# Performance work log

Measured on AMD Instinct MI355X. Metric: run time of the kernel, lower is better.

The kernel has to match this reference:

```python
import jax, jax.numpy as jnp
import numpy as np

B, N, D, H, E, K = 8, 4096, 128, 256, 16, 2


def setup_inputs() -> dict:
    key = jax.random.key(0)
    ks = jax.random.split(key, 11)
    sc = 0.05
    return {
        "x":   jax.random.normal(ks[0], (B, N, D), jnp.float32),
        "Wg":  jax.random.normal(ks[1], (D, E), jnp.float32) * sc,
        "bg":  jnp.zeros((E,), jnp.float32),
        "W1":  jax.random.normal(ks[2], (E, D, H), jnp.float32) * sc,
        "b1":  jnp.zeros((E, H), jnp.float32),
        "W2":  jax.random.normal(ks[3], (E, H, D), jnp.float32) * sc,
        "b2":  jnp.zeros((E, D), jnp.float32),
        "Wu1": jax.random.normal(ks[4], (D, H), jnp.float32) * sc,
        "bu1": jnp.zeros((H,), jnp.float32),
        "Wu2": jax.random.normal(ks[5], (H, D), jnp.float32) * sc,
        "bu2": jnp.zeros((D,), jnp.float32),
    }


def reference(x, Wg, bg, W1, b1, W2, b2, Wu1, bu1, Wu2, bu2):
    b, n, d = x.shape
    xt = x.reshape(b * n, d)                       # [T, D]
    T = xt.shape[0]

    # gating: top-k logits kept, rest -inf, then softmax -> zeros off top-k
    logits = xt @ Wg + bg                          # [T, E]
    topv, topi = jax.lax.top_k(logits, K)          # [T, K]
    mask = jnp.full_like(logits, -jnp.inf)
    mask = mask.at[jnp.arange(T)[:, None], topi].set(topv)
    gate = jax.nn.softmax(mask, axis=-1)           # [T, E]

    # dense all-expert MLP (matches original torch.stack over experts)
    h = jax.nn.relu(jnp.einsum('td,edh->teh', xt, W1) + b1)   # [T, E, H]
    eo = jnp.einsum('teh,ehd->ted', h, W2) + b2               # [T, E, D]

    # universal expert scaled by omega = 1 - max gate
    omega = 1.0 - jnp.max(gate, axis=1, keepdims=True)        # [T, 1]
    uni = omega * (jax.nn.relu(xt @ Wu1 + bu1) @ Wu2 + bu2)   # [T, D]

    out = jnp.einsum('te,ted->td', gate, eo) + uni
    return out.reshape(b, n, d)
```

## Files before the change

### kernel.cpp

```cpp
#include <hip/hip_runtime.h>
#include <hip/hip_bf16.h>

constexpr int kT = 32768;
constexpr int kD = 128;
constexpr int kH = 256;
constexpr int kE = 16;

typedef __bf16 bf16x8 __attribute__((ext_vector_type(8)));
typedef unsigned short u16x8 __attribute__((ext_vector_type(8)));
typedef float f32x4 __attribute__((ext_vector_type(4)));

#define LDX 136
#define LDQ 72

constexpr int NB_TP   = 272;
constexpr int NB_GATE = kT / 64;
constexpr int CNT_STRIDE = 32;
constexpr int MOE_GRID = 1552;

__device__ __forceinline__ unsigned short f2bf(float f) {
  unsigned int u = __float_as_uint(f);
  u += 0x7FFFu + ((u >> 16) & 1u);
  return (unsigned short)(u >> 16);
}
__device__ __forceinline__ float bf2f(unsigned short s) {
  return __uint_as_float((unsigned int)s << 16);
}
__device__ __forceinline__ void bar_lgkm() {
  asm volatile("s_waitcnt lgkmcnt(0)" ::: "memory");
  __builtin_amdgcn_s_barrier();
  asm volatile("" ::: "memory");
}

__global__ __launch_bounds__(256) void front_kernel(
    const float* __restrict__ x, const float* __restrict__ Wg,
    const float* __restrict__ bg,
    const float* __restrict__ W1, const float* __restrict__ W2,
    const float* __restrict__ Wu1, const float* __restrict__ Wu2,
    unsigned short* __restrict__ xb, unsigned short* __restrict__ W1t,
    unsigned short* __restrict__ W2t, unsigned short* __restrict__ Wu1t,
    unsigned short* __restrict__ Wu2t,
    int* __restrict__ cnt, int* __restrict__ btok, float* __restrict__ bgate,
    int* __restrict__ tpos)
{
  __shared__ __align__(16) char smem[46848];
  const int tid = threadIdx.x;
  const int b = blockIdx.x;

  if (b < NB_TP) {
    int bb = b;
    const float* src; unsigned short* dst; int R, C, r0, c0;
    if (bb < 136) {
      int m = bb >> 3, t8 = bb & 7;
      R = 128; C = 256;
      src = (m < 16) ? W1 + (size_t)m * 32768 : Wu1;
      dst = (m < 16) ? W1t + (size_t)m * 32768 : Wu1t;
      r0 = (t8 & 1) * 64; c0 = (t8 >> 1) * 64;
    } else {
      bb -= 136;
      int m = bb >> 3, t8 = bb & 7;
      R = 256; C = 128;
      src = (m < 16) ? W2 + (size_t)m * 32768 : Wu2;
      dst = (m < 16) ? W2t + (size_t)m * 32768 : Wu2t;
      r0 = (t8 >> 1) * 64; c0 = (t8 & 1) * 64;
    }
    unsigned short (*tl)[72] = reinterpret_cast<unsigned short(*)[72]>(smem);
#pragma unroll
    for (int i = 0; i < 4; ++i) {
      int s = i * 256 + tid;
      int r = s >> 4, c4 = s & 15;
      float4 v = *reinterpret_cast<const float4*>(&src[(size_t)(r0 + r) * C + c0 + c4 * 4]);
      tl[c4 * 4 + 0][r] = f2bf(v.x);
      tl[c4 * 4 + 1][r] = f2bf(v.y);
      tl[c4 * 4 + 2][r] = f2bf(v.z);
      tl[c4 * 4 + 3][r] = f2bf(v.w);
    }
    __syncthreads();
#pragma unroll
    for (int i = 0; i < 2; ++i) {
      int s = i * 256 + tid;
      int c = s >> 3, seg = s & 7;
      uint4 v = *reinterpret_cast<const uint4*>(&tl[c][seg * 8]);
      *reinterpret_cast<uint4*>(&dst[(size_t)(c0 + c) * R + r0 + seg * 8]) = v;
    }
    return;
  }

  {
    float* sWt = reinterpret_cast<float*>(smem);
    float* sX  = reinterpret_cast<float*>(smem + 8448);
    float* sL  = reinterpret_cast<float*>(smem + 42240);
    int* hcnt  = reinterpret_cast<int*>(smem + 46592);
    int* hbase = reinterpret_cast<int*>(smem + 46656);
    int* hb16  = reinterpret_cast<int*>(smem + 46720);
    const int t0 = (b - NB_TP) * 64;

    if (tid < kE) hcnt[tid] = 0;
    for (int i = tid; i < kD * kE; i += 256) {
      int d = i >> 4, e = i & 15;
      sWt[e * 132 + d] = Wg[i];
    }
    const float4* xv = reinterpret_cast<const float4*>(x + (size_t)t0 * kD);
    for (int i = tid; i < 64 * kD / 4; i += 256) {
      int r = i >> 5, c4 = i & 31;
      *reinterpret_cast<float4*>(&sX[r * 132 + c4 * 4]) = xv[i];
    }
    __syncthreads();

    const int e = tid & 15, tq = tid >> 4;
    const double bgd = (double)bg[e];
    const float4* wr = reinterpret_cast<const float4*>(&sWt[e * 132]);
    double acc[4] = {0.0, 0.0, 0.0, 0.0};
#pragma unroll
    for (int d4 = 0; d4 < 32; ++d4) {
      float4 wa = wr[d4];
#pragma unroll
      for (int p = 0; p < 4; ++p) {
        float4 xa = *reinterpret_cast<const float4*>(&sX[(p * 16 + tq) * 132 + d4 * 4]);
        acc[p] += (double)xa.x * (double)wa.x + (double)xa.y * (double)wa.y
                + (double)xa.z * (double)wa.z + (double)xa.w * (double)wa.w;
      }
    }
#pragma unroll
    for (int p = 0; p < 4; ++p)
      sL[(p * 16 + tq) * 17 + e] = (float)(acc[p] + bgd);
#pragma unroll
    for (int p = 0; p < 4; ++p) {
      int idx = p * 256 + tid;
      int r = idx >> 4, c8 = (idx & 15) * 8;
      const float* sp = &sX[r * 132 + c8];
      u16x8 v;
#pragma unroll
      for (int j = 0; j < 8; ++j) v[j] = f2bf(sp[j]);
      *reinterpret_cast<u16x8*>(&xb[(size_t)(t0 + r) * kD + c8]) = v;
    }
    __syncthreads();

    int e0 = 0, e1 = 0, lp0 = 0, lp1 = 0;
    float g0 = 0.f, g1 = 0.f;
    const int t = t0 + tid;
    if (tid < 64) {
      float v0 = -3.4e38f, v1 = -3.4e38f;
      for (int i = 0; i < kE; ++i) {
        float v = sL[tid * 17 + i];
        if (v > v0) { v1 = v0; e1 = e0; v0 = v; e0 = i; }
        else if (v > v1) { v1 = v; e1 = i; }
      }
      float r = expf(v1 - v0);
      g0 = 1.f / (1.f + r);
      g1 = 1.f - g0;
      lp0 = atomicAdd(&hcnt[e0], 1);
      lp1 = atomicAdd(&hcnt[e1], 1);
    }
    if (tid == 0) hb16[0] = atomicAdd(&cnt[16 * CNT_STRIDE], 64);
    __syncthreads();
    if (tid < kE)
      hbase[tid] = atomicAdd(&cnt[tid * CNT_STRIDE], hcnt[tid]);
    __syncthreads();
    if (tid < 64) {
      int p0 = hbase[e0] + lp0;
      btok[e0 * kT + p0] = t; bgate[e0 * kT + p0] = g0;
      int p1 = hbase[e1] + lp1;
      btok[e1 * kT + p1] = t; bgate[e1 * kT + p1] = g1;
      int p2 = hb16[0] + tid;
      btok[16 * kT + p2] = t; bgate[16 * kT + p2] = 1.f - g0;
      tpos[2 * t]     = (e0 << 16) | p0;
      tpos[2 * t + 1] = (e1 << 16) | p1;
    }
  }
}

#define LOAD_W1(BUF, HQ)                                                      \
  _Pragma("unroll")                                                           \
  for (int kk = 0; kk < 4; ++kk)                                              \
    W1r[BUF][kk] = *reinterpret_cast<const bf16x8*>(                          \
        Bw1 + (size_t)((HQ) * 64 + w * 16 + lr) * kD + kk * 32 + lg * 8);

#define LOAD_W2(BUF, HQ)                                                      \
  _Pragma("unroll")                                                           \
  for (int n = 0; n < 2; ++n)                                                 \
    _Pragma("unroll")                                                         \
    for (int k2 = 0; k2 < 2; ++k2)                                            \
      W2r[BUF][n * 2 + k2] = *reinterpret_cast<const bf16x8*>(                \
          Bw2 + (size_t)(w * 32 + n * 16 + lr) * kH + (HQ) * 64 + k2 * 32 + lg * 8);

__global__ __launch_bounds__(256) void moe_kernel(
    const unsigned short* __restrict__ xb,
    const unsigned short* __restrict__ W1t,
    const unsigned short* __restrict__ W2t,
    const unsigned short* __restrict__ Wu1t,
    const unsigned short* __restrict__ Wu2t,
    const float* __restrict__ b1, const float* __restrict__ b2,
    const float* __restrict__ bu1, const float* __restrict__ bu2,
    const int* __restrict__ cnt, const int* __restrict__ btok,
    const float* __restrict__ bgate,
    unsigned short* __restrict__ eo, float* __restrict__ out)
{
  __shared__ alignas(16) char smem[27136];
  unsigned short* xs = reinterpret_cast<unsigned short*>(smem);
  unsigned short* hs = reinterpret_cast<unsigned short*>(smem + 17408);
  int*   toks = reinterpret_cast<int*>(smem + 26624);
  float* gts  = reinterpret_cast<float*>(smem + 26880);
  unsigned short* stB = reinterpret_cast<unsigned short*>(smem);
  float* stF = reinterpret_cast<float*>(smem);
  const int tid = threadIdx.x;
  const int bid = blockIdx.x;

  int c17[17];
#pragma unroll
  for (int i = 0; i < 17; ++i) c17[i] = cnt[i * CNT_STRIDE];
  int e = -1, tile = 0, eobase = 0, accb = 0;
#pragma unroll
  for (int i = 0; i < 17; ++i) {
    int tl = (c17[i] + 63) >> 6;
    if (e < 0) {
      if (bid < accb + tl) { e = i; tile = bid - accb; }
      else { accb += tl; if (i < 16) eobase += c17[i]; }
    }
  }
  if (e < 0) return;
  const int rows = min(64, c17[e] - tile * 64);

  const int w = tid >> 6, l = tid & 63, lr = l & 15, lg = l >> 4;
  const int gr = tid >> 4, gc = (tid & 15) * 8;
  const f32x4 z4 = {0.f, 0.f, 0.f, 0.f};

  const unsigned short* Bw1 = (e < 16) ? W1t + (size_t)e * kH * kD : Wu1t;
  const unsigned short* Bw2 = (e < 16) ? W2t + (size_t)e * kD * kH : Wu2t;
  const float* bs1 = (e < 16) ? b1 + (size_t)e * kH : bu1;
  const float* bs2 = (e < 16) ? b2 + (size_t)e * kD : bu2;

  bf16x8 W1r[2][4], W2r[2][4];
  LOAD_W1(0, 0); LOAD_W2(0, 0);
  float b1q[4];
#pragma unroll
  for (int hq = 0; hq < 4; ++hq) b1q[hq] = bs1[hq * 64 + w * 16 + lr];
  float b2v[2];
#pragma unroll
  for (int n = 0; n < 2; ++n) b2v[n] = bs2[w * 32 + n * 16 + lr];

  {
    int tokR[4]; float gtR[4];
#pragma unroll
    for (int p = 0; p < 4; ++p) {
      int r = p * 16 + gr; bool v = r < rows; int bi2 = e * kT + tile * 64 + r;
      tokR[p] = v ? btok[bi2] : 0;
      gtR[p]  = v ? bgate[bi2] : 0.f;
    }
#pragma unroll
    for (int p = 0; p < 4; ++p) {
      uint4 v = *reinterpret_cast<const uint4*>(xb + (size_t)tokR[p] * kD + gc);
      *reinterpret_cast<uint4*>(&xs[(p * 16 + gr) * LDX + gc]) = v;
    }
    if ((tid & 15) == 0) {
#pragma unroll
      for (int p = 0; p < 4; ++p) {
        toks[p * 16 + gr] = tokR[p];
        gts[p * 16 + gr]  = gtR[p];
      }
    }
  }
  f32x4 acc2[4][2];
#pragma unroll
  for (int m = 0; m < 4; ++m)
#pragma unroll
    for (int n = 0; n < 2; ++n) acc2[m][n] = z4;
  bar_lgkm();

#pragma unroll
  for (int hq = 0; hq < 4; ++hq) {
    const int cur = hq & 1;
    if (hq < 3) {
      const int nxt = cur ^ 1;
      LOAD_W1(nxt, hq + 1);
      LOAD_W2(nxt, hq + 1);
    }
    f32x4 acc[4];
#pragma unroll
    for (int m = 0; m < 4; ++m) acc[m] = z4;
#pragma unroll
    for (int kk = 0; kk < 4; ++kk) {
      bf16x8 a[4];
#pragma unroll
      for (int m = 0; m < 4; ++m)
        a[m] = *reinterpret_cast<const bf16x8*>(xs + (m * 16 + lr) * LDX + kk * 32 + lg * 8);
#pragma unroll
      for (int m = 0; m < 4; ++m)
        acc[m] = __builtin_amdgcn_mfma_f32_16x16x32_bf16(a[m], W1r[cur][kk], acc[m], 0, 0, 0);
    }
#pragma unroll
    for (int m = 0; m < 4; ++m)
#pragma unroll
      for (int q = 0; q < 4; ++q) {
        float v = acc[m][q] + b1q[hq];
        v = fmaxf(v, 0.f);
        hs[(m * 16 + lg * 4 + q) * LDQ + w * 16 + lr] = f2bf(v);
      }
    bar_lgkm();
#pragma unroll
    for (int k2 = 0; k2 < 2; ++k2) {
      bf16x8 a[4];
#pragma unroll
      for (int m = 0; m < 4; ++m)
        a[m] = *reinterpret_cast<const bf16x8*>(hs + (m * 16 + lr) * LDQ + k2 * 32 + lg * 8);
#pragma unroll
      for (int m = 0; m < 4; ++m)
#pragma unroll
        for (int n = 0; n < 2; ++n)
          acc2[m][n] = __builtin_amdgcn_mfma_f32_16x16x32_bf16(a[m], W2r[cur][n * 2 + k2], acc2[m][n], 0, 0, 0);
    }
    bar_lgkm();
  }

  if (e < 16) {
#pragma unroll
    for (int m = 0; m < 4; ++m)
#pragma unroll
      for (int q = 0; q < 4; ++q) {
        int r = m * 16 + lg * 4 + q;
        float g = gts[r];
#pragma unroll
        for (int n = 0; n < 2; ++n)
          stB[r * LDX + w * 32 + n * 16 + lr] = f2bf(g * (acc2[m][n][q] + b2v[n]));
      }
    bar_lgkm();
    unsigned short* dst = eo + (size_t)(eobase + tile * 64) * kD;
#pragma unroll
    for (int j = 0; j < 4; ++j) {
      int gidx = j * 256 + tid;
      int r = gidx >> 4, seg = gidx & 15;
      if (r < rows) {
        uint4 v = *reinterpret_cast<const uint4*>(&stB[r * LDX + seg * 8]);
        *reinterpret_cast<uint4*>(dst + (size_t)r * kD + seg * 8) = v;
      }
    }
  } else {
#pragma unroll
    for (int ch = 0; ch < 2; ++ch) {
      if ((w >> 1) == ch) {
#pragma unroll
        for (int m = 0; m < 4; ++m)
#pragma unroll
          for (int q = 0; q < 4; ++q) {
            int r = m * 16 + lg * 4 + q;
            float g = gts[r];
#pragma unroll
            for (int n = 0; n < 2; ++n)
              stF[r * 68 + (w & 1) * 32 + n * 16 + lr] = g * (acc2[m][n][q] + b2v[n]);
          }
      }
      bar_lgkm();
#pragma unroll
      for (int j = 0; j < 4; ++j) {
        int gidx = j * 256 + tid;
        int r = gidx >> 4, seg = gidx & 15;
        if (r < rows) {
          int tok = toks[r];
          float4 v = *reinterpret_cast<const float4*>(&stF[r * 68 + seg * 4]);
          *reinterpret_cast<float4*>(out + (size_t)tok * kD + ch * 64 + seg * 4) = v;
        }
      }
      bar_lgkm();
    }
  }
}

__global__ __launch_bounds__(256) void combine_kernel(
    const int* __restrict__ cnt, const int* __restrict__ tpos,
    const unsigned short* __restrict__ eo, float* __restrict__ out)
{
  __shared__ int base[16];
  const int tid = threadIdx.x;
  if (tid < 16) {
    int s = 0;
    for (int i = 0; i < tid; ++i) s += cnt[i * CNT_STRIDE];
    base[tid] = s;
  }
  __syncthreads();
  const int tk = blockIdx.x * 16 + (tid >> 4);
  const int c = tid & 15;
  int a0 = tpos[2 * tk], a1 = tpos[2 * tk + 1];
  size_t r0 = (size_t)(base[a0 >> 16] + (a0 & 0xffff)) * kD + c * 8;
  size_t r1 = (size_t)(base[a1 >> 16] + (a1 & 0xffff)) * kD + c * 8;
  u16x8 v0 = *reinterpret_cast<const u16x8*>(eo + r0);
  u16x8 v1 = *reinterpret_cast<const u16x8*>(eo + r1);
  float s[8];
#pragma unroll
  for (int j = 0; j < 8; ++j) s[j] = bf2f(v0[j]) + bf2f(v1[j]);
  float4* op = reinterpret_cast<float4*>(out + (size_t)tk * kD + c * 8);
  float4 o0 = op[0], o1 = op[1];
  o0.x += s[0]; o0.y += s[1]; o0.z += s[2]; o0.w += s[3];
  o1.x += s[4]; o1.y += s[5]; o1.z += s[6]; o1.w += s[7];
  op[0] = o0; op[1] = o1;
}

extern "C" void kernel_launch(void* const* d_in, const int* in_sizes, int n_in,
                              void* d_out, int out_size, void* d_ws, size_t ws_size,
                              hipStream_t stream) {
  (void)in_sizes; (void)n_in; (void)out_size; (void)ws_size;
  const float* x   = (const float*)d_in[0];
  const float* Wg  = (const float*)d_in[1];
  const float* bg  = (const float*)d_in[2];
  const float* W1  = (const float*)d_in[3];
  const float* b1  = (const float*)d_in[4];
  const float* W2  = (const float*)d_in[5];
  const float* b2  = (const float*)d_in[6];
  const float* Wu1 = (const float*)d_in[7];
  const float* bu1 = (const float*)d_in[8];
  const float* Wu2 = (const float*)d_in[9];
  const float* bu2 = (const float*)d_in[10];
  float* out = (float*)d_out;

  char* ws = (char*)d_ws;
  constexpr size_t OFF_XB    = 0;
  constexpr size_t OFF_W1T   = 8388608;
  constexpr size_t OFF_W2T   = 9437184;
  constexpr size_t OFF_WU1T  = 10485760;
  constexpr size_t OFF_WU2T  = 10551296;
  constexpr size_t OFF_CNT   = 10616832;
  constexpr size_t OFF_TPOS  = 10620928;
  constexpr size_t OFF_BTOK  = 10883072;
  constexpr size_t OFF_BGATE = 13111296;
  constexpr size_t OFF_EO    = 15339520;

  unsigned short* xb   = (unsigned short*)(ws + OFF_XB);
  unsigned short* W1t  = (unsigned short*)(ws + OFF_W1T);
  unsigned short* W2t  = (unsigned short*)(ws + OFF_W2T);
  unsigned short* Wu1t = (unsigned short*)(ws + OFF_WU1T);
  unsigned short* Wu2t = (unsigned short*)(ws + OFF_WU2T);
  int*   cnt   = (int*)(ws + OFF_CNT);
  int*   tpos  = (int*)(ws + OFF_TPOS);
  int*   btok  = (int*)(ws + OFF_BTOK);
  float* bgate = (float*)(ws + OFF_BGATE);
  unsigned short* eo = (unsigned short*)(ws + OFF_EO);

  hipMemsetAsync(cnt, 0, 17 * CNT_STRIDE * sizeof(int), stream);
  front_kernel<<<NB_TP + NB_GATE, 256, 0, stream>>>(
      x, Wg, bg, W1, W2, Wu1, Wu2,
      xb, W1t, W2t, Wu1t, Wu2t, cnt, btok, bgate, tpos);
  moe_kernel<<<MOE_GRID, 256, 0, stream>>>(
      xb, W1t, W2t, Wu1t, Wu2t, b1, b2, bu1, bu2, cnt, btok, bgate, eo, out);
  combine_kernel<<<kT / 16, 256, 0, stream>>>(cnt, tpos, eo, out);
}
```

Measured before the change: 76.06 us.

## Swap MFMA operands for transposed accumulators and remap block ids across XCDs

Swaps the A/B operands of both MFMA GEMMs so each lane's accumulator holds four consecutive columns of one row instead of four rows of one column. The bias adds, ReLU and bf16/f32 writes to shared memory become single vectorized 8- or 16-byte stores per fragment instead of scalar stores. Bias loads become f32x4 vector loads, and the gate is read once per m-tile. Block ids are also permuted so that consecutive work tiles, which share expert weights, land on the same XCD for better L2 reuse; this assumes the grid size is divisible by 8.

```diff
diff --git a/kernel.cpp b/kernel.cpp
--- a/kernel.cpp
+++ b/kernel.cpp
@@ -8,6 +8,7 @@
 
 typedef __bf16 bf16x8 __attribute__((ext_vector_type(8)));
 typedef unsigned short u16x8 __attribute__((ext_vector_type(8)));
+typedef unsigned short u16x4 __attribute__((ext_vector_type(4)));
 typedef float f32x4 __attribute__((ext_vector_type(4)));
 
 #define LDX 136
@@ -204,7 +205,7 @@
   unsigned short* stB = reinterpret_cast<unsigned short*>(smem);
   float* stF = reinterpret_cast<float*>(smem);
   const int tid = threadIdx.x;
-  const int bid = blockIdx.x;
+  const int bid = (blockIdx.x & 7) * (MOE_GRID / 8) + (blockIdx.x >> 3);
 
   int c17[17];
 #pragma unroll
@@ -232,12 +233,13 @@
 
   bf16x8 W1r[2][4], W2r[2][4];
   LOAD_W1(0, 0); LOAD_W2(0, 0);
-  float b1q[4];
-#pragma unroll
-  for (int hq = 0; hq < 4; ++hq) b1q[hq] = bs1[hq * 64 + w * 16 + lr];
-  float b2v[2];
-#pragma unroll
-  for (int n = 0; n < 2; ++n) b2v[n] = bs2[w * 32 + n * 16 + lr];
+  f32x4 b1s[4], b2s[2];
+#pragma unroll
+  for (int hq = 0; hq < 4; ++hq)
+    b1s[hq] = *reinterpret_cast<const f32x4*>(bs1 + hq * 64 + w * 16 + lg * 4);
+#pragma unroll
+  for (int n = 0; n < 2; ++n)
+    b2s[n] = *reinterpret_cast<const f32x4*>(bs2 + w * 32 + n * 16 + lg * 4);
 
   {
     int tokR[4]; float gtR[4];
@@ -286,16 +288,16 @@
         a[m] = *reinterpret_cast<const bf16x8*>(xs + (m * 16 + lr) * LDX + kk * 32 + lg * 8);
 #pragma unroll
       for (int m = 0; m < 4; ++m)
-        acc[m] = __builtin_amdgcn_mfma_f32_16x16x32_bf16(a[m], W1r[cur][kk], acc[m], 0, 0, 0);
-    }
-#pragma unroll
-    for (int m = 0; m < 4; ++m)
-#pragma unroll
-      for (int q = 0; q < 4; ++q) {
-        float v = acc[m][q] + b1q[hq];
-        v = fmaxf(v, 0.f);
-        hs[(m * 16 + lg * 4 + q) * LDQ + w * 16 + lr] = f2bf(v);
-      }
+        acc[m] = __builtin_amdgcn_mfma_f32_16x16x32_bf16(W1r[cur][kk], a[m], acc[m], 0, 0, 0);
+    }
+#pragma unroll
+    for (int m = 0; m < 4; ++m) {
+      u16x4 hv;
+#pragma unroll
+      for (int q = 0; q < 4; ++q)
+        hv[q] = f2bf(fmaxf(acc[m][q] + b1s[hq][q], 0.f));
+      *reinterpret_cast<u16x4*>(&hs[(m * 16 + lr) * LDQ + w * 16 + lg * 4]) = hv;
+    }
     bar_lgkm();
 #pragma unroll
     for (int k2 = 0; k2 < 2; ++k2) {
@@ -307,22 +309,24 @@
       for (int m = 0; m < 4; ++m)
 #pragma unroll
         for (int n = 0; n < 2; ++n)
-          acc2[m][n] = __builtin_amdgcn_mfma_f32_16x16x32_bf16(a[m], W2r[cur][n * 2 + k2], acc2[m][n], 0, 0, 0);
+          acc2[m][n] = __builtin_amdgcn_mfma_f32_16x16x32_bf16(W2r[cur][n * 2 + k2], a[m], acc2[m][n], 0, 0, 0);
     }
     bar_lgkm();
   }
 
   if (e < 16) {
 #pragma unroll
-    for (int m = 0; m < 4; ++m)
-#pragma unroll
-      for (int q = 0; q < 4; ++q) {
-        int r = m * 16 + lg * 4 + q;
-        float g = gts[r];
-#pragma unroll
-        for (int n = 0; n < 2; ++n)
-          stB[r * LDX + w * 32 + n * 16 + lr] = f2bf(g * (acc2[m][n][q] + b2v[n]));
-      }
+    for (int m = 0; m < 4; ++m) {
+      float g = gts[m * 16 + lr];
+#pragma unroll
+      for (int n = 0; n < 2; ++n) {
+        u16x4 sv;
+#pragma unroll
+        for (int q = 0; q < 4; ++q)
+          sv[q] = f2bf(g * (acc2[m][n][q] + b2s[n][q]));
+        *reinterpret_cast<u16x4*>(&stB[(m * 16 + lr) * LDX + w * 32 + n * 16 + lg * 4]) = sv;
+      }
+    }
     bar_lgkm();
     unsigned short* dst = eo + (size_t)(eobase + tile * 64) * kD;
 #pragma unroll
@@ -339,15 +343,17 @@
     for (int ch = 0; ch < 2; ++ch) {
       if ((w >> 1) == ch) {
 #pragma unroll
-        for (int m = 0; m < 4; ++m)
-#pragma unroll
-          for (int q = 0; q < 4; ++q) {
-            int r = m * 16 + lg * 4 + q;
-            float g = gts[r];
-#pragma unroll
-            for (int n = 0; n < 2; ++n)
-              stF[r * 68 + (w & 1) * 32 + n * 16 + lr] = g * (acc2[m][n][q] + b2v[n]);
+        for (int m = 0; m < 4; ++m) {
+          float g = gts[m * 16 + lr];
+#pragma unroll
+          for (int n = 0; n < 2; ++n) {
+            f32x4 sv;
+#pragma unroll
+            for (int q = 0; q < 4; ++q)
+              sv[q] = g * (acc2[m][n][q] + b2s[n][q]);
+            *reinterpret_cast<f32x4*>(&stF[(m * 16 + lr) * 68 + (w & 1) * 32 + n * 16 + lg * 4]) = sv;
           }
+        }
       }
       bar_lgkm();
 #pragma unroll
```

Measured after the change: 79.71 us. 4.8% more time.

## Split universal expert into its own kernel fused with the combine step

Applied to the files above, without the earlier changes.

The universal expert moves out of the routed MoE kernel into a new kernel that processes contiguous 64-token tiles. That kernel computes omega-scaled universal MLP output and adds the two gathered expert rows before writing out directly. This removes the separate combine kernel's read-modify-write of the fp32 output and the scattered writes of the universal-expert path. The trade-off is one extra omega buffer and a smaller expert grid, while keeping three launches in total.

```diff
diff --git a/kernel.cpp b/kernel.cpp
--- a/kernel.cpp
+++ b/kernel.cpp
@@ -8,6 +8,7 @@
 
 typedef __bf16 bf16x8 __attribute__((ext_vector_type(8)));
 typedef unsigned short u16x8 __attribute__((ext_vector_type(8)));
+typedef unsigned short u16x4 __attribute__((ext_vector_type(4)));
 typedef float f32x4 __attribute__((ext_vector_type(4)));
 
 #define LDX 136
@@ -16,7 +17,7 @@
 constexpr int NB_TP   = 272;
 constexpr int NB_GATE = kT / 64;
 constexpr int CNT_STRIDE = 32;
-constexpr int MOE_GRID = 1552;
+constexpr int EXP_GRID = 1040;
 
 __device__ __forceinline__ unsigned short f2bf(float f) {
   unsigned int u = __float_as_uint(f);
@@ -41,7 +42,7 @@
     unsigned short* __restrict__ W2t, unsigned short* __restrict__ Wu1t,
     unsigned short* __restrict__ Wu2t,
     int* __restrict__ cnt, int* __restrict__ btok, float* __restrict__ bgate,
-    int* __restrict__ tpos)
+    int* __restrict__ tpos, float* __restrict__ omega)
 {
   __shared__ __align__(16) char smem[46848];
   const int tid = threadIdx.x;
@@ -92,7 +93,6 @@
     float* sL  = reinterpret_cast<float*>(smem + 42240);
     int* hcnt  = reinterpret_cast<int*>(smem + 46592);
     int* hbase = reinterpret_cast<int*>(smem + 46656);
-    int* hb16  = reinterpret_cast<int*>(smem + 46720);
     const int t0 = (b - NB_TP) * 64;
 
     if (tid < kE) hcnt[tid] = 0;
@@ -149,10 +149,10 @@
       float r = expf(v1 - v0);
       g0 = 1.f / (1.f + r);
       g1 = 1.f - g0;
+      omega[t] = 1.f - g0;
       lp0 = atomicAdd(&hcnt[e0], 1);
       lp1 = atomicAdd(&hcnt[e1], 1);
     }
-    if (tid == 0) hb16[0] = atomicAdd(&cnt[16 * CNT_STRIDE], 64);
     __syncthreads();
     if (tid < kE)
       hbase[tid] = atomicAdd(&cnt[tid * CNT_STRIDE], hcnt[tid]);
@@ -162,8 +162,6 @@
       btok[e0 * kT + p0] = t; bgate[e0 * kT + p0] = g0;
       int p1 = hbase[e1] + lp1;
       btok[e1 * kT + p1] = t; bgate[e1 * kT + p1] = g1;
-      int p2 = hb16[0] + tid;
-      btok[16 * kT + p2] = t; bgate[16 * kT + p2] = 1.f - g0;
       tpos[2 * t]     = (e0 << 16) | p0;
       tpos[2 * t + 1] = (e1 << 16) | p1;
     }
@@ -184,17 +182,14 @@
       W2r[BUF][n * 2 + k2] = *reinterpret_cast<const bf16x8*>(                \
           Bw2 + (size_t)(w * 32 + n * 16 + lr) * kH + (HQ) * 64 + k2 * 32 + lg * 8);
 
-__global__ __launch_bounds__(256) void moe_kernel(
+__global__ __launch_bounds__(256) void moe_expert_kernel(
     const unsigned short* __restrict__ xb,
     const unsigned short* __restrict__ W1t,
     const unsigned short* __restrict__ W2t,
-    const unsigned short* __restrict__ Wu1t,
-    const unsigned short* __restrict__ Wu2t,
     const float* __restrict__ b1, const float* __restrict__ b2,
-    const float* __restrict__ bu1, const float* __restrict__ bu2,
     const int* __restrict__ cnt, const int* __restrict__ btok,
     const float* __restrict__ bgate,
-    unsigned short* __restrict__ eo, float* __restrict__ out)
+    unsigned short* __restrict__ eo)
 {
   __shared__ alignas(16) char smem[27136];
   unsigned short* xs = reinterpret_cast<unsigned short*>(smem);
@@ -202,33 +197,32 @@
   int*   toks = reinterpret_cast<int*>(smem + 26624);
   float* gts  = reinterpret_cast<float*>(smem + 26880);
   unsigned short* stB = reinterpret_cast<unsigned short*>(smem);
-  float* stF = reinterpret_cast<float*>(smem);
   const int tid = threadIdx.x;
   const int bid = blockIdx.x;
 
-  int c17[17];
-#pragma unroll
-  for (int i = 0; i < 17; ++i) c17[i] = cnt[i * CNT_STRIDE];
+  int c16[16];
+#pragma unroll
+  for (int i = 0; i < 16; ++i) c16[i] = cnt[i * CNT_STRIDE];
   int e = -1, tile = 0, eobase = 0, accb = 0;
 #pragma unroll
-  for (int i = 0; i < 17; ++i) {
-    int tl = (c17[i] + 63) >> 6;
+  for (int i = 0; i < 16; ++i) {
+    int tl = (c16[i] + 63) >> 6;
     if (e < 0) {
       if (bid < accb + tl) { e = i; tile = bid - accb; }
-      else { accb += tl; if (i < 16) eobase += c17[i]; }
+      else { accb += tl; eobase += c16[i]; }
     }
   }
   if (e < 0) return;
-  const int rows = min(64, c17[e] - tile * 64);
+  const int rows = min(64, c16[e] - tile * 64);
 
   const int w = tid >> 6, l = tid & 63, lr = l & 15, lg = l >> 4;
   const int gr = tid >> 4, gc = (tid & 15) * 8;
   const f32x4 z4 = {0.f, 0.f, 0.f, 0.f};
 
-  const unsigned short* Bw1 = (e < 16) ? W1t + (size_t)e * kH * kD : Wu1t;
-  const unsigned short* Bw2 = (e < 16) ? W2t + (size_t)e * kD * kH : Wu2t;
-  const float* bs1 = (e < 16) ? b1 + (size_t)e * kH : bu1;
-  const float* bs2 = (e < 16) ? b2 + (size_t)e * kD : bu2;
+  const unsigned short* Bw1 = W1t + (size_t)e * kH * kD;
+  const unsigned short* Bw2 = W2t + (size_t)e * kD * kH;
+  const float* bs1 = b1 + (size_t)e * kH;
+  const float* bs2 = b2 + (size_t)e * kD;
 
   bf16x8 W1r[2][4], W2r[2][4];
   LOAD_W1(0, 0); LOAD_W2(0, 0);
@@ -312,86 +306,160 @@
     bar_lgkm();
   }
 
-  if (e < 16) {
+#pragma unroll
+  for (int m = 0; m < 4; ++m)
+#pragma unroll
+    for (int q = 0; q < 4; ++q) {
+      int r = m * 16 + lg * 4 + q;
+      float g = gts[r];
+#pragma unroll
+      for (int n = 0; n < 2; ++n)
+        stB[r * LDX + w * 32 + n * 16 + lr] = f2bf(g * (acc2[m][n][q] + b2v[n]));
+    }
+  bar_lgkm();
+  unsigned short* dst = eo + (size_t)(eobase + tile * 64) * kD;
+#pragma unroll
+  for (int j = 0; j < 4; ++j) {
+    int gidx = j * 256 + tid;
+    int r = gidx >> 4, seg = gidx & 15;
+    if (r < rows) {
+      uint4 v = *reinterpret_cast<const uint4*>(&stB[r * LDX + seg * 8]);
+      *reinterpret_cast<uint4*>(dst + (size_t)r * kD + seg * 8) = v;
+    }
+  }
+}
+
+__global__ __launch_bounds__(256) void uni_combine_kernel(
+    const unsigned short* __restrict__ xb,
+    const unsigned short* __restrict__ Wu1t,
+    const unsigned short* __restrict__ Wu2t,
+    const float* __restrict__ bu1, const float* __restrict__ bu2,
+    const float* __restrict__ omega, const int* __restrict__ cnt,
+    const int* __restrict__ tpos, const unsigned short* __restrict__ eo,
+    float* __restrict__ out)
+{
+  __shared__ alignas(16) char smem[27456];
+  unsigned short* xs = reinterpret_cast<unsigned short*>(smem);
+  unsigned short* hs = reinterpret_cast<unsigned short*>(smem + 17408);
+  float* sOm  = reinterpret_cast<float*>(smem + 26624);
+  int*   sTp  = reinterpret_cast<int*>(smem + 26880);
+  int*   sBase= reinterpret_cast<int*>(smem + 27392);
+  float* stF  = reinterpret_cast<float*>(smem);
+  const int tid = threadIdx.x;
+  const int t0 = blockIdx.x * 64;
+
+  const int w = tid >> 6, l = tid & 63, lr = l & 15, lg = l >> 4;
+  const int gr = tid >> 4, gc = (tid & 15) * 8;
+  const f32x4 z4 = {0.f, 0.f, 0.f, 0.f};
+
+  const unsigned short* Bw1 = Wu1t;
+  const unsigned short* Bw2 = Wu2t;
+  bf16x8 W1r[2][4], W2r[2][4];
+  LOAD_W1(0, 0); LOAD_W2(0, 0);
+  float b1q[4];
+#pragma unroll
+  for (int hq = 0; hq < 4; ++hq) b1q[hq] = bu1[hq * 64 + w * 16 + lr];
+  float b2v[2];
+#pragma unroll
+  for (int n = 0; n < 2; ++n) b2v[n] = bu2[w * 32 + n * 16 + lr];
+
+  if (tid < 16) {
+    int s = 0;
+    for (int i = 0; i < tid; ++i) s += cnt[i * CNT_STRIDE];
+    sBase[tid] = s;
+  }
+  if (tid >= 64 && tid < 128) sOm[tid - 64] = omega[t0 + tid - 64];
+  if (tid >= 128) sTp[tid - 128] = tpos[2 * t0 + tid - 128];
+#pragma unroll
+  for (int p = 0; p < 4; ++p) {
+    uint4 v = *reinterpret_cast<const uint4*>(xb + (size_t)(t0 + p * 16 + gr) * kD + gc);
+    *reinterpret_cast<uint4*>(&xs[(p * 16 + gr) * LDX + gc]) = v;
+  }
+  f32x4 acc2[4][2];
+#pragma unroll
+  for (int m = 0; m < 4; ++m)
+#pragma unroll
+    for (int n = 0; n < 2; ++n) acc2[m][n] = z4;
+  bar_lgkm();
+
+#pragma unroll
+  for (int hq = 0; hq < 4; ++hq) {
+    const int cur = hq & 1;
+    if (hq < 3) {
+      const int nxt = cur ^ 1;
+      LOAD_W1(nxt, hq + 1);
+      LOAD_W2(nxt, hq + 1);
+    }
+    f32x4 acc[4];
+#pragma unroll
+    for (int m = 0; m < 4; ++m) acc[m] = z4;
+#pragma unroll
+    for (int kk = 0; kk < 4; ++kk) {
+      bf16x8 a[4];
+#pragma unroll
+      for (int m = 0; m < 4; ++m)
+        a[m] = *reinterpret_cast<const bf16x8*>(xs + (m * 16 + lr) * LDX + kk * 32 + lg * 8);
+#pragma unroll
+      for (int m = 0; m < 4; ++m)
+        acc[m] = __builtin_amdgcn_mfma_f32_16x16x32_bf16(a[m], W1r[cur][kk], acc[m], 0, 0, 0);
+    }
 #pragma unroll
     for (int m = 0; m < 4; ++m)
 #pragma unroll
       for (int q = 0; q < 4; ++q) {
-        int r = m * 16 + lg * 4 + q;
-        float g = gts[r];
-#pragma unroll
-        for (int n = 0; n < 2; ++n)
-          stB[r * LDX + w * 32 + n * 16 + lr] = f2bf(g * (acc2[m][n][q] + b2v[n]));
+        float v = acc[m][q] + b1q[hq];
+        v = fmaxf(v, 0.f);
+        hs[(m * 16 + lg * 4 + q) * LDQ + w * 16 + lr] = f2bf(v);
       }
     bar_lgkm();
-    unsigned short* dst = eo + (size_t)(eobase + tile * 64) * kD;
+#pragma unroll
+    for (int k2 = 0; k2 < 2; ++k2) {
+      bf16x8 a[4];
+#pragma unroll
+      for (int m = 0; m < 4; ++m)
+        a[m] = *reinterpret_cast<const bf16x8*>(hs + (m * 16 + lr) * LDQ + k2 * 32 + lg * 8);
+#pragma unroll
+      for (int m = 0; m < 4; ++m)
+#pragma unroll
+        for (int n = 0; n < 2; ++n)
+          acc2[m][n] = __builtin_amdgcn_mfma_f32_16x16x32_bf16(a[m], W2r[cur][n * 2 + k2], acc2[m][n], 0, 0, 0);
+    }
+    bar_lgkm();
+  }
+
+#pragma unroll
+  for (int ch = 0; ch < 2; ++ch) {
+    if ((w >> 1) == ch) {
+#pragma unroll
+      for (int m = 0; m < 4; ++m)
+#pragma unroll
+        for (int q = 0; q < 4; ++q) {
+          int r = m * 16 + lg * 4 + q;
+          float om = sOm[r];
+#pragma unroll
+          for (int n = 0; n < 2; ++n)
+            stF[r * 68 + (w & 1) * 32 + n * 16 + lr] = om * (acc2[m][n][q] + b2v[n]);
+        }
+    }
+    bar_lgkm();
 #pragma unroll
     for (int j = 0; j < 4; ++j) {
       int gidx = j * 256 + tid;
       int r = gidx >> 4, seg = gidx & 15;
-      if (r < rows) {
-        uint4 v = *reinterpret_cast<const uint4*>(&stB[r * LDX + seg * 8]);
-        *reinterpret_cast<uint4*>(dst + (size_t)r * kD + seg * 8) = v;
-      }
-    }
-  } else {
-#pragma unroll
-    for (int ch = 0; ch < 2; ++ch) {
-      if ((w >> 1) == ch) {
-#pragma unroll
-        for (int m = 0; m < 4; ++m)
-#pragma unroll
-          for (int q = 0; q < 4; ++q) {
-            int r = m * 16 + lg * 4 + q;
-            float g = gts[r];
-#pragma unroll
-            for (int n = 0; n < 2; ++n)
-              stF[r * 68 + (w & 1) * 32 + n * 16 + lr] = g * (acc2[m][n][q] + b2v[n]);
-          }
-      }
-      bar_lgkm();
-#pragma unroll
-      for (int j = 0; j < 4; ++j) {
-        int gidx = j * 256 + tid;
-        int r = gidx >> 4, seg = gidx & 15;
-        if (r < rows) {
-          int tok = toks[r];
-          float4 v = *reinterpret_cast<const float4*>(&stF[r * 68 + seg * 4]);
-          *reinterpret_cast<float4*>(out + (size_t)tok * kD + ch * 64 + seg * 4) = v;
-        }
-      }
-      bar_lgkm();
-    }
-  }
-}
-
-__global__ __launch_bounds__(256) void combine_kernel(
-    const int* __restrict__ cnt, const int* __restrict__ tpos,
-    const unsigned short* __restrict__ eo, float* __restrict__ out)
-{
-  __shared__ int base[16];
-  const int tid = threadIdx.x;
-  if (tid < 16) {
-    int s = 0;
-    for (int i = 0; i < tid; ++i) s += cnt[i * CNT_STRIDE];
-    base[tid] = s;
-  }
-  __syncthreads();
-  const int tk = blockIdx.x * 16 + (tid >> 4);
-  const int c = tid & 15;
-  int a0 = tpos[2 * tk], a1 = tpos[2 * tk + 1];
-  size_t r0 = (size_t)(base[a0 >> 16] + (a0 & 0xffff)) * kD + c * 8;
-  size_t r1 = (size_t)(base[a1 >> 16] + (a1 & 0xffff)) * kD + c * 8;
-  u16x8 v0 = *reinterpret_cast<const u16x8*>(eo + r0);
-  u16x8 v1 = *reinterpret_cast<const u16x8*>(eo + r1);
-  float s[8];
-#pragma unroll
-  for (int j = 0; j < 8; ++j) s[j] = bf2f(v0[j]) + bf2f(v1[j]);
-  float4* op = reinterpret_cast<float4*>(out + (size_t)tk * kD + c * 8);
-  float4 o0 = op[0], o1 = op[1];
-  o0.x += s[0]; o0.y += s[1]; o0.z += s[2]; o0.w += s[3];
-  o1.x += s[4]; o1.y += s[5]; o1.z += s[6]; o1.w += s[7];
-  op[0] = o0; op[1] = o1;
+      int a0 = sTp[2 * r], a1 = sTp[2 * r + 1];
+      size_t e0r = (size_t)(sBase[a0 >> 16] + (a0 & 0xffff)) * kD + ch * 64 + seg * 4;
+      size_t e1r = (size_t)(sBase[a1 >> 16] + (a1 & 0xffff)) * kD + ch * 64 + seg * 4;
+      u16x4 v0 = *reinterpret_cast<const u16x4*>(eo + e0r);
+      u16x4 v1 = *reinterpret_cast<const u16x4*>(eo + e1r);
+      float4 v = *reinterpret_cast<const float4*>(&stF[r * 68 + seg * 4]);
+      v.x += bf2f(v0[0]) + bf2f(v1[0]);
+      v.y += bf2f(v0[1]) + bf2f(v1[1]);
+      v.z += bf2f(v0[2]) + bf2f(v1[2]);
+      v.w += bf2f(v0[3]) + bf2f(v1[3]);
+      *reinterpret_cast<float4*>(out + (size_t)(t0 + r) * kD + ch * 64 + seg * 4) = v;
+    }
+    bar_lgkm();
+  }
 }
 
 extern "C" void kernel_launch(void* const* d_in, const int* in_sizes, int n_in,
@@ -422,6 +490,7 @@
   constexpr size_t OFF_BTOK  = 10883072;
   constexpr size_t OFF_BGATE = 13111296;
   constexpr size_t OFF_EO    = 15339520;
+  constexpr size_t OFF_OM    = 32116736;
 
   unsigned short* xb   = (unsigned short*)(ws + OFF_XB);
   unsigned short* W1t  = (unsigned short*)(ws + OFF_W1T);
@@ -433,12 +502,14 @@
   int*   btok  = (int*)(ws + OFF_BTOK);
   float* bgate = (float*)(ws + OFF_BGATE);
   unsigned short* eo = (unsigned short*)(ws + OFF_EO);
-
-  hipMemsetAsync(cnt, 0, 17 * CNT_STRIDE * sizeof(int), stream);
+  float* omega = (float*)(ws + OFF_OM);
+
+  hipMemsetAsync(cnt, 0, kE * CNT_STRIDE * sizeof(int), stream);
   front_kernel<<<NB_TP + NB_GATE, 256, 0, stream>>>(
       x, Wg, bg, W1, W2, Wu1, Wu2,
-      xb, W1t, W2t, Wu1t, Wu2t, cnt, btok, bgate, tpos);
-  moe_kernel<<<MOE_GRID, 256, 0, stream>>>(
-      xb, W1t, W2t, Wu1t, Wu2t, b1, b2, bu1, bu2, cnt, btok, bgate, eo, out);
-  combine_kernel<<<kT / 16, 256, 0, stream>>>(cnt, tpos, eo, out);
-}
+      xb, W1t, W2t, Wu1t, Wu2t, cnt, btok, bgate, tpos, omega);
+  moe_expert_kernel<<<EXP_GRID, 256, 0, stream>>>(
+      xb, W1t, W2t, b1, b2, cnt, btok, bgate, eo);
+  uni_combine_kernel<<<kT / 64, 256, 0, stream>>>(
+      xb, Wu1t, Wu2t, bu1, bu2, omega, cnt, tpos, eo, out);
+}
```

Result: faster. 69.27 us, median of 3 (-8.9%).
